# Kernel optimization log

Hardware: AMD Instinct MI355X
Metric: run time of the kernel (lower is better)

## Reference

```python
import jax, jax.numpy as jnp
import numpy as np

N = 50000
E = 800000
D = 256
EPS = 1e-5  # BatchNorm eps


def _gcn_conv(x, W, b, row, col):
    # PyG GCNConv: h = x @ W; add self-loops; sym-normalize; scatter-add; + bias
    h = x @ W  # [N, D]
    deg = jnp.zeros((N,), x.dtype).at[col].add(jnp.ones((row.shape[0],), x.dtype))
    dinv = jax.lax.rsqrt(deg)  # deg >= 1 thanks to self-loops
    norm = dinv[row] * dinv[col]  # [E+N]
    msg = h[row] * norm[:, None]  # gather + scale, [E+N, D]
    out = jnp.zeros_like(h).at[col].add(msg)  # scatter-aggregate
    return out + b


def _bn(x, gamma, beta):
    # BatchNorm1d in training mode: batch statistics over nodes
    m = jnp.mean(x, axis=0)
    v = jnp.var(x, axis=0)
    return (x - m) * jax.lax.rsqrt(v + EPS) * gamma + beta


def setup_inputs() -> dict:
    key = jax.random.key(0)
    ks = jax.random.split(key, 4)
    x = jax.random.normal(ks[0], (N, D), dtype=jnp.float32)
    edge_index = jax.random.randint(ks[1], (2, E), 0, N, dtype=jnp.int64)
    s = 1.0 / np.sqrt(D)
    W1 = jax.random.uniform(ks[2], (D, D), jnp.float32, -s, s)
    W2 = jax.random.uniform(ks[3], (D, D), jnp.float32, -s, s)
    z = jnp.zeros((D,), jnp.float32)
    o = jnp.ones((D,), jnp.float32)
    return {"x": x, "edge_index": edge_index,
            "W1": W1, "b1": z, "g1": o, "be1": z,
            "W2": W2, "b2": z, "g2": o, "be2": z}


def reference(x, edge_index, W1, b1, g1, be1, W2, b2, g2, be2):
    loops = jnp.arange(N, dtype=edge_index.dtype)
    row = jnp.concatenate([edge_index[0], loops])  # sources
    col = jnp.concatenate([edge_index[1], loops])  # targets
    # layer 1: GCNConv -> BN -> ReLU (dropout is identity in eval)
    h = _gcn_conv(x, W1, b1, row, col)
    h = jax.nn.relu(_bn(h, g1, be1))
    # layer 2
    h = _gcn_conv(h, W2, b2, row, col)
    h = jax.nn.relu(_bn(h, g2, be2))
    return h
```

## Files before the change

kernel.cpp:

```cpp
#include <hip/hip_runtime.h>
#include <cstdint>
#include <cstddef>

constexpr int N = 50000;
constexpr int E = 800000;
constexpr int D = 256;
constexpr float EPS = 1e-5f;
constexpr int NB = (N + 255) / 256;
constexpr int GB = (N + 63) / 64;
constexpr int CB = (E + 255) / 256;
constexpr int AGG_BLOCKS = 2048;

constexpr int ZTOT4 = (N * 4 + 4 * D * 4 + 16) / 16;
constexpr int ZBLK = (ZTOT4 + 63) / 64;

typedef __attribute__((ext_vector_type(8))) short short8;
typedef __attribute__((ext_vector_type(4))) float f32x4;

__device__ __forceinline__ unsigned short f2bf(float f) {
  union { float f; unsigned u; } c; c.f = f;
  unsigned u = c.u;
  u += 0x7fff + ((u >> 16) & 1);
  return (unsigned short)(u >> 16);
}
__device__ __forceinline__ float bf2f(unsigned short h) {
  union { unsigned u; float f; } c; c.u = ((unsigned)h) << 16;
  return c.f;
}
__device__ __forceinline__ float bflo(unsigned u) {
  union { unsigned x; float f; } c; c.x = u << 16; return c.f;
}
__device__ __forceinline__ float bfhi(unsigned u) {
  union { unsigned x; float f; } c; c.x = u & 0xffff0000u; return c.f;
}
__device__ __forceinline__ unsigned cvt_pk(float lo, float hi) {
  unsigned r;
  asm("v_cvt_pk_bf16_f32 %0, %1, %2" : "=v"(r) : "v"(lo), "v"(hi));
  return r;
}
__device__ __forceinline__ int2 ldnt_pair(const int2* p) {
  unsigned long long v = __builtin_nontemporal_load((const unsigned long long*)p);
  int2 r;
  r.x = (int)(unsigned)(v & 0xffffffffull);
  r.y = (int)(unsigned)(v >> 32);
  return r;
}

__device__ __forceinline__ int detect64(const void* ei) {
  const int* p = (const int*)ei;
  int l = threadIdx.x & 63;
  int nz = (p[2 * l + 1] != 0) | (p[2 * l + 129] != 0);
  return __ballot(nz) == 0ULL;
}

__device__ __forceinline__ int edge_at(const void* ei, int is64, long long pos) {
  if (is64) return (int)((const long long*)ei)[pos];
  return ((const int*)ei)[pos];
}

template <bool A_BF16, bool FUSE_BN>
__device__ __forceinline__ void gemm_body(const void* __restrict__ Ap,
                                          const unsigned short* __restrict__ Wf,
                                          unsigned short* __restrict__ C,
                                          const float* __restrict__ sc,
                                          const float* __restrict__ sh,
                                          int bid) {
  __shared__ unsigned short As[64][264];
  int t = threadIdx.x;
  int lane = t & 63;
  int w = t >> 6;
  int row0 = bid * 64;
  int l16 = lane & 15, lk = lane >> 4;

  f32x4 acc[4][4];
#pragma unroll
  for (int i = 0; i < 4; ++i)
#pragma unroll
    for (int j = 0; j < 4; ++j) acc[i][j] = (f32x4){0.f, 0.f, 0.f, 0.f};

  int arow = t >> 2;
  int ak0 = (t & 3) * 8;
  int gr = row0 + arow;
  bool inb = (gr < N);

#pragma unroll
  for (int ks = 0; ks < 8; ++ks) {
    int kc = ks * 32 + ak0;
    float f[8] = {0.f, 0.f, 0.f, 0.f, 0.f, 0.f, 0.f, 0.f};
    if (inb) {
      if (A_BF16) {
        const unsigned short* A = (const unsigned short*)Ap;
        short8 v = *(const short8*)&A[(size_t)gr * 256 + kc];
#pragma unroll
        for (int j = 0; j < 8; ++j) f[j] = bf2f((unsigned short)v[j]);
      } else {
        const float* A = (const float*)Ap;
        float4 f0 = *(const float4*)&A[(size_t)gr * 256 + kc];
        float4 f1 = *(const float4*)&A[(size_t)gr * 256 + kc + 4];
        f[0] = f0.x; f[1] = f0.y; f[2] = f0.z; f[3] = f0.w;
        f[4] = f1.x; f[5] = f1.y; f[6] = f1.z; f[7] = f1.w;
      }
    }
    if (FUSE_BN) {
#pragma unroll
      for (int j = 0; j < 8; ++j)
        f[j] = fmaxf(fmaf(f[j], sc[kc + j], sh[kc + j]), 0.f);
    }
    uint4 pk;
    pk.x = cvt_pk(f[0], f[1]);
    pk.y = cvt_pk(f[2], f[3]);
    pk.z = cvt_pk(f[4], f[5]);
    pk.w = cvt_pk(f[6], f[7]);
    *(uint4*)&As[arow][kc] = pk;
  }
  __syncthreads();

#pragma unroll
  for (int ks = 0; ks < 8; ++ks) {
    short8 af[4];
#pragma unroll
    for (int mf = 0; mf < 4; ++mf)
      af[mf] = *(const short8*)&As[mf * 16 + l16][ks * 32 + lk * 8];
#pragma unroll
    for (int nf = 0; nf < 4; ++nf) {
      short8 bf = *(const short8*)&Wf[(((size_t)ks * 16 + w * 4 + nf) * 64 + lane) * 8];
#pragma unroll
      for (int mf = 0; mf < 4; ++mf)
        acc[mf][nf] = __builtin_amdgcn_mfma_f32_16x16x32_bf16(af[mf], bf, acc[mf][nf], 0, 0, 0);
    }
  }
  __syncthreads();

  unsigned short(*Cs)[264] = As;
#pragma unroll
  for (int mf = 0; mf < 4; ++mf)
#pragma unroll
    for (int nf = 0; nf < 4; ++nf)
#pragma unroll
      for (int r = 0; r < 4; ++r)
        Cs[mf * 16 + lk * 4 + r][w * 64 + nf * 16 + l16] = f2bf(acc[mf][nf][r]);
  __syncthreads();
#pragma unroll
  for (int it = 0; it < 8; ++it) {
    int r = it * 8 + (t >> 5);
    int gr2 = row0 + r;
    if (gr2 < N)
      *(short8*)&C[(size_t)gr2 * 256 + (t & 31) * 8] = *(const short8*)&Cs[r][(t & 31) * 8];
  }
}

__global__ __launch_bounds__(256) void k_gemm1_count(const float* __restrict__ x,
                                                     const unsigned short* __restrict__ Wf1,
                                                     unsigned short* __restrict__ hbuf,
                                                     const void* __restrict__ ei,
                                                     int* __restrict__ degc) {
  if (blockIdx.x < GB) {
    gemm_body<false, false>(x, Wf1, hbuf, nullptr, nullptr, blockIdx.x);
  } else {
    int is64 = detect64(ei);
    int e = (blockIdx.x - GB) * 256 + threadIdx.x;
    if (e >= E) return;
    int c = edge_at(ei, is64, (long long)E + e);
    atomicAdd(&degc[c], 1);
  }
}

__global__ __launch_bounds__(256) void k_gemm2(const unsigned short* __restrict__ A,
                                               const unsigned short* __restrict__ Wf,
                                               unsigned short* __restrict__ C,
                                               const float* __restrict__ sc,
                                               const float* __restrict__ sh) {
  gemm_body<true, true>(A, Wf, C, sc, sh, blockIdx.x);
}

__global__ void k_scan_partial(const int* __restrict__ degc, int* __restrict__ bsum,
                               float* __restrict__ dinv) {
  __shared__ int sd[256];
  int t = threadIdx.x;
  int i = blockIdx.x * 256 + t;
  int dv = (i < N) ? degc[i] : 0;
  if (i < N) dinv[i] = rsqrtf((float)(dv + 1));
  int v = (i < N) ? (dv + 1) : 0;
  sd[t] = v;
  __syncthreads();
  for (int s = 128; s > 0; s >>= 1) {
    if (t < s) sd[t] += sd[t + s];
    __syncthreads();
  }
  if (t == 0) bsum[blockIdx.x] = sd[0];
}

__global__ void k_scan_final(const int* __restrict__ degc, const int* __restrict__ bsum,
                             const float* __restrict__ dinv, int* __restrict__ offs,
                             int* __restrict__ curs, int2* __restrict__ epair) {
  __shared__ int sb[256];
  __shared__ int sd[256];
  int t = threadIdx.x;
  int bv = (t < NB) ? bsum[t] : 0;
  sb[t] = bv;
  __syncthreads();
  for (int off = 1; off < 256; off <<= 1) {
    int x = (t >= off) ? sb[t - off] : 0;
    __syncthreads();
    sb[t] += x;
    __syncthreads();
  }
  int base = sb[blockIdx.x] - bsum[blockIdx.x];
  int i = blockIdx.x * 256 + t;
  int v = (i < N) ? (degc[i] + 1) : 0;
  sd[t] = v;
  __syncthreads();
  for (int off = 1; off < 256; off <<= 1) {
    int x = (t >= off) ? sd[t - off] : 0;
    __syncthreads();
    sd[t] += x;
    __syncthreads();
  }
  if (i < N) {
    int o = base + sd[t] - v;
    offs[i] = o;
    curs[i] = o + 1;
    float d = dinv[i];
    epair[o] = make_int2(i, __float_as_int(d * d));
  }
  if (i == N - 1) offs[N] = base + sd[t];
}

__global__ void k_fill_edges(const void* __restrict__ ei,
                             const float* __restrict__ dinv, int* __restrict__ curs,
                             int2* __restrict__ epair) {
  int is64 = detect64(ei);
  int e = blockIdx.x * 256 + threadIdx.x;
  if (e >= E) return;
  int r = edge_at(ei, is64, e);
  int c = edge_at(ei, is64, (long long)E + e);
  int p = atomicAdd(&curs[c], 1);
  epair[p] = make_int2(r, __float_as_int(dinv[r] * dinv[c]));
}

__global__ void k_wfrag(const float* __restrict__ W1, const float* __restrict__ W2,
                        unsigned short* __restrict__ Wf1, unsigned short* __restrict__ Wf2,
                        int4* __restrict__ zbase) {
  int b = blockIdx.x;
  if (b >= 256) {
    int idx4 = (b - 256) * 64 + threadIdx.x;
    if (idx4 < ZTOT4) zbase[idx4] = make_int4(0, 0, 0, 0);
    return;
  }
  const float* W = (b < 128) ? W1 : W2;
  unsigned short* Wf = (b < 128) ? Wf1 : Wf2;
  int tile = b & 127;
  int lane = threadIdx.x;
  int kstep = tile >> 4, wn = tile & 15;
  int kbase = kstep * 32 + (lane >> 4) * 8;
  int col = wn * 16 + (lane & 15);
  float f[8];
#pragma unroll
  for (int j = 0; j < 8; ++j) f[j] = W[(size_t)(kbase + j) * 256 + col];
  uint4 pk;
  pk.x = cvt_pk(f[0], f[1]);
  pk.y = cvt_pk(f[2], f[3]);
  pk.z = cvt_pk(f[4], f[5]);
  pk.w = cvt_pk(f[6], f[7]);
  *(uint4*)&Wf[(((size_t)tile) * 64 + lane) * 8] = pk;
}

__global__ __launch_bounds__(256) void k_agg(const unsigned short* __restrict__ h,
                                             const int* __restrict__ offs,
                                             const int2* __restrict__ epair,
                                             const float* __restrict__ bias,
                                             unsigned short* __restrict__ outp,
                                             float* __restrict__ partial) {
  int t = threadIdx.x;
  int wv = t >> 6;
  int lane = t & 63;
  float4 bb = ((const float4*)bias)[lane];
  float s0 = 0.f, s1 = 0.f, s2 = 0.f, s3 = 0.f;
  float q0 = 0.f, q1 = 0.f, q2 = 0.f, q3 = 0.f;

#define ACC4(v, wgt)                         \
  do {                                       \
    a0 = fmaf(wgt, bflo((v).x), a0);         \
    a1 = fmaf(wgt, bfhi((v).x), a1);         \
    a2 = fmaf(wgt, bflo((v).y), a2);         \
    a3 = fmaf(wgt, bfhi((v).y), a3);         \
  } while (0)

  for (int nd0 = blockIdx.x * 4; nd0 < N; nd0 += AGG_BLOCKS * 4) {
    int nd = nd0 + wv;
    if (nd < N) {
      int node = __builtin_amdgcn_readfirstlane(nd);
      int e = offs[node];
      int end = offs[node + 1];
      float a0 = 0.f, a1 = 0.f, a2 = 0.f, a3 = 0.f;

      for (; e + 8 <= end; e += 8) {
        int2 p0 = ldnt_pair(&epair[e + 0]), p1 = ldnt_pair(&epair[e + 1]);
        int2 p2 = ldnt_pair(&epair[e + 2]), p3 = ldnt_pair(&epair[e + 3]);
        int2 p4 = ldnt_pair(&epair[e + 4]), p5 = ldnt_pair(&epair[e + 5]);
        int2 p6 = ldnt_pair(&epair[e + 6]), p7 = ldnt_pair(&epair[e + 7]);
        uint2 v0 = *(const uint2*)&h[(size_t)p0.x * 256 + lane * 4];
        uint2 v1 = *(const uint2*)&h[(size_t)p1.x * 256 + lane * 4];
        uint2 v2 = *(const uint2*)&h[(size_t)p2.x * 256 + lane * 4];
        uint2 v3 = *(const uint2*)&h[(size_t)p3.x * 256 + lane * 4];
        uint2 v4 = *(const uint2*)&h[(size_t)p4.x * 256 + lane * 4];
        uint2 v5 = *(const uint2*)&h[(size_t)p5.x * 256 + lane * 4];
        uint2 v6 = *(const uint2*)&h[(size_t)p6.x * 256 + lane * 4];
        uint2 v7 = *(const uint2*)&h[(size_t)p7.x * 256 + lane * 4];
        ACC4(v0, __int_as_float(p0.y));
        ACC4(v1, __int_as_float(p1.y));
        ACC4(v2, __int_as_float(p2.y));
        ACC4(v3, __int_as_float(p3.y));
        ACC4(v4, __int_as_float(p4.y));
        ACC4(v5, __int_as_float(p5.y));
        ACC4(v6, __int_as_float(p6.y));
        ACC4(v7, __int_as_float(p7.y));
      }
      if (e < end) {
#pragma unroll
        for (int k = 0; k < 8; ++k) {
          int idx = e + k;
          bool act = (idx < end);
          int2 p = ldnt_pair(&epair[act ? idx : end - 1]);
          float wgt = act ? __int_as_float(p.y) : 0.f;
          uint2 v = *(const uint2*)&h[(size_t)p.x * 256 + lane * 4];
          ACC4(v, wgt);
        }
      }

      uint2 ov;
      ov.x = cvt_pk(a0 + bb.x, a1 + bb.y);
      ov.y = cvt_pk(a2 + bb.z, a3 + bb.w);
      *(uint2*)&outp[(size_t)nd * 256 + lane * 4] = ov;
      float f0 = bflo(ov.x), f1 = bfhi(ov.x), f2v = bflo(ov.y), f3 = bfhi(ov.y);
      s0 += f0; q0 = fmaf(f0, f0, q0);
      s1 += f1; q1 = fmaf(f1, f1, q1);
      s2 += f2v; q2 = fmaf(f2v, f2v, q2);
      s3 += f3; q3 = fmaf(f3, f3, q3);
    }
  }
#undef ACC4

  __shared__ float4 ps[256];
  __shared__ float4 pq[256];
  ps[t] = {s0, s1, s2, s3};
  pq[t] = {q0, q1, q2, q3};
  __syncthreads();
  float* pout = partial + (size_t)blockIdx.x * 512;
  if (t < 64) {
    float4 a = ps[t], b = ps[64 + t], c = ps[128 + t], d = ps[192 + t];
    float4 o = {a.x + b.x + c.x + d.x, a.y + b.y + c.y + d.y,
                a.z + b.z + c.z + d.z, a.w + b.w + c.w + d.w};
    ((float4*)pout)[t] = o;
  } else if (t < 128) {
    int l = t - 64;
    float4 a = pq[l], b = pq[64 + l], c = pq[128 + l], d = pq[192 + l];
    float4 o = {a.x + b.x + c.x + d.x, a.y + b.y + c.y + d.y,
                a.z + b.z + c.z + d.z, a.w + b.w + c.w + d.w};
    ((float4*)(pout + 256))[l] = o;
  }
}

__global__ __launch_bounds__(256) void k_bnred(const float* __restrict__ partial,
                                               float* __restrict__ bnsum,
                                               float* __restrict__ bnsq,
                                               int* __restrict__ cnt,
                                               const float* __restrict__ g,
                                               const float* __restrict__ be,
                                               float* __restrict__ sc,
                                               float* __restrict__ sh) {
  int t = threadIdx.x;
  float s = 0.f, q = 0.f;
  int b0 = blockIdx.x * (AGG_BLOCKS / 16);
  for (int b = b0; b < b0 + AGG_BLOCKS / 16; ++b) {
    s += partial[(size_t)b * 512 + t];
    q += partial[(size_t)b * 512 + 256 + t];
  }
  atomicAdd(&bnsum[t], s);
  atomicAdd(&bnsq[t], q);
  __threadfence();
  __shared__ int last;
  if (t == 0) last = (atomicAdd(cnt, 1) == 15);
  __syncthreads();
  if (last) {
    float S = atomicAdd(&bnsum[t], 0.f);
    float Q = atomicAdd(&bnsq[t], 0.f);
    const float inv = 1.f / (float)N;
    float m = S * inv;
    float v = Q * inv - m * m;
    float sf = rsqrtf(v + EPS) * g[t];
    sc[t] = sf;
    sh[t] = be[t] - m * sf;
  }
}

__global__ __launch_bounds__(256) void k_bnapply(const unsigned short* __restrict__ in,
                                                 float* __restrict__ outp,
                                                 const float* __restrict__ sc,
                                                 const float* __restrict__ sh) {
  int t = threadIdx.x;
  int lane = t & 63;
  int sub = t >> 6;
  float4 s4 = ((const float4*)sc)[lane];
  float4 h4 = ((const float4*)sh)[lane];
  for (int r = blockIdx.x * 4 + sub; r < N; r += gridDim.x * 4) {
    uint2 u = *(const uint2*)&in[(size_t)r * 256 + lane * 4];
    float4 v;
    v.x = fmaxf(fmaf(bflo(u.x), s4.x, h4.x), 0.f);
    v.y = fmaxf(fmaf(bfhi(u.x), s4.y, h4.y), 0.f);
    v.z = fmaxf(fmaf(bflo(u.y), s4.z, h4.z), 0.f);
    v.w = fmaxf(fmaf(bfhi(u.y), s4.w, h4.w), 0.f);
    *(float4*)&outp[(size_t)r * 256 + lane * 4] = v;
  }
}

extern "C" void kernel_launch(void* const* d_in, const int* in_sizes, int n_in,
                              void* d_out, int out_size, void* d_ws, size_t ws_size,
                              hipStream_t stream) {
  const float* x  = (const float*)d_in[0];
  const void*  ei = d_in[1];
  const float* W1 = (const float*)d_in[2];
  const float* b1 = (const float*)d_in[3];
  const float* g1 = (const float*)d_in[4];
  const float* be1 = (const float*)d_in[5];
  const float* W2 = (const float*)d_in[6];
  const float* b2 = (const float*)d_in[7];
  const float* g2 = (const float*)d_in[8];
  const float* be2 = (const float*)d_in[9];
  float* out = (float*)d_out;

  char* base = (char*)d_ws;
  size_t off = 0;
  unsigned short* hbuf = (unsigned short*)(base + off); off += (size_t)N * D * 2;
  unsigned short* abuf = (unsigned short*)(base + off); off += (size_t)N * D * 2;
  unsigned short* Wf1 = (unsigned short*)(base + off);  off += (size_t)D * D * 2;
  unsigned short* Wf2 = (unsigned short*)(base + off);  off += (size_t)D * D * 2;
  int*   degc = (int*)(base + off);    off += (size_t)N * 4;
  float* bnsum1 = (float*)(base + off); off += (size_t)D * 4;
  float* bnsq1  = (float*)(base + off); off += (size_t)D * 4;
  float* bnsum2 = (float*)(base + off); off += (size_t)D * 4;
  float* bnsq2  = (float*)(base + off); off += (size_t)D * 4;
  int*   cnt1 = (int*)(base + off);    off += 8;
  int*   cnt2 = (int*)(base + off);    off += 8;
  float* dinv = (float*)(base + off); off += (size_t)N * 4;
  int*   offs = (int*)(base + off);   off += (size_t)(N + 4) * 4;
  int*   curs = (int*)(base + off);   off += (size_t)N * 4;
  int2*  epair = (int2*)(base + off); off += (size_t)(E + N) * 8;
  float* partial = (float*)(base + off); off += (size_t)AGG_BLOCKS * 512 * 4;
  float* sc1 = (float*)(base + off);  off += (size_t)D * 4;
  float* sh1 = (float*)(base + off);  off += (size_t)D * 4;
  float* sc2 = (float*)(base + off);  off += (size_t)D * 4;
  float* sh2 = (float*)(base + off);  off += (size_t)D * 4;
  int*   bsum = (int*)(base + off);   off += 256 * 4;

  k_wfrag<<<256 + ZBLK, 64, 0, stream>>>(W1, W2, Wf1, Wf2, (int4*)degc);

  k_gemm1_count<<<GB + CB, 256, 0, stream>>>(x, Wf1, hbuf, ei, degc);

  k_scan_partial<<<NB, 256, 0, stream>>>(degc, bsum, dinv);
  k_scan_final<<<NB, 256, 0, stream>>>(degc, bsum, dinv, offs, curs, epair);
  k_fill_edges<<<CB, 256, 0, stream>>>(ei, dinv, curs, epair);

  k_agg<<<AGG_BLOCKS, 256, 0, stream>>>(hbuf, offs, epair, b1, abuf, partial);
  k_bnred<<<16, 256, 0, stream>>>(partial, bnsum1, bnsq1, cnt1, g1, be1, sc1, sh1);

  k_gemm2<<<GB, 256, 0, stream>>>(abuf, Wf2, hbuf, sc1, sh1);
  k_agg<<<AGG_BLOCKS, 256, 0, stream>>>(hbuf, offs, epair, b2, abuf, partial);
  k_bnred<<<16, 256, 0, stream>>>(partial, bnsum2, bnsq2, cnt2, g2, be2, sc2, sh2);
  k_bnapply<<<512, 256, 0, stream>>>(abuf, out, sc2, sh2);
}
```

Baseline: 280.4 us.

## Merge scan kernels with grid barrier and move degree count into wfrag

Replaces the zeroing blocks with hipMemsetAsync and moves the degree-count atomics into the weight-fragment kernel, so GEMM1 runs alone. The two scan kernels are merged into one with a spin-wait grid barrier on a done counter, which removes a launch and reuses the computed dinv. The final BN-apply output uses nontemporal stores. The spin barrier assumes all NB (196) blocks are co-resident, which holds on this GPU but is fragile. The done counter sits inside the memset range so it is reset on every call.

```diff
diff --git a/kernel.cpp b/kernel.cpp
--- a/kernel.cpp
+++ b/kernel.cpp
@@ -9,10 +9,8 @@
 constexpr int NB = (N + 255) / 256;
 constexpr int GB = (N + 63) / 64;
 constexpr int CB = (E + 255) / 256;
+constexpr int CB64 = (E + 63) / 64;
 constexpr int AGG_BLOCKS = 2048;
-
-constexpr int ZTOT4 = (N * 4 + 4 * D * 4 + 16) / 16;
-constexpr int ZBLK = (ZTOT4 + 63) / 64;
 
 typedef __attribute__((ext_vector_type(8))) short short8;
 typedef __attribute__((ext_vector_type(4))) float f32x4;
@@ -149,20 +147,10 @@
   }
 }
 
-__global__ __launch_bounds__(256) void k_gemm1_count(const float* __restrict__ x,
-                                                     const unsigned short* __restrict__ Wf1,
-                                                     unsigned short* __restrict__ hbuf,
-                                                     const void* __restrict__ ei,
-                                                     int* __restrict__ degc) {
-  if (blockIdx.x < GB) {
-    gemm_body<false, false>(x, Wf1, hbuf, nullptr, nullptr, blockIdx.x);
-  } else {
-    int is64 = detect64(ei);
-    int e = (blockIdx.x - GB) * 256 + threadIdx.x;
-    if (e >= E) return;
-    int c = edge_at(ei, is64, (long long)E + e);
-    atomicAdd(&degc[c], 1);
-  }
+__global__ __launch_bounds__(256) void k_gemm1(const float* __restrict__ x,
+                                               const unsigned short* __restrict__ Wf,
+                                               unsigned short* __restrict__ C) {
+  gemm_body<false, false>(x, Wf, C, nullptr, nullptr, blockIdx.x);
 }
 
 __global__ __launch_bounds__(256) void k_gemm2(const unsigned short* __restrict__ A,
@@ -173,29 +161,67 @@
   gemm_body<true, true>(A, Wf, C, sc, sh, blockIdx.x);
 }
 
-__global__ void k_scan_partial(const int* __restrict__ degc, int* __restrict__ bsum,
-                               float* __restrict__ dinv) {
+__global__ __launch_bounds__(64) void k_wfrag_count(
+    const float* __restrict__ W1, const float* __restrict__ W2,
+    unsigned short* __restrict__ Wf1, unsigned short* __restrict__ Wf2,
+    const void* __restrict__ ei, int* __restrict__ degc) {
+  int b = blockIdx.x;
+  if (b >= 256) {
+    int is64 = detect64(ei);
+    int e = (b - 256) * 64 + threadIdx.x;
+    if (e >= E) return;
+    int c = edge_at(ei, is64, (long long)E + e);
+    atomicAdd(&degc[c], 1);
+    return;
+  }
+  const float* W = (b < 128) ? W1 : W2;
+  unsigned short* Wf = (b < 128) ? Wf1 : Wf2;
+  int tile = b & 127;
+  int lane = threadIdx.x;
+  int kstep = tile >> 4, wn = tile & 15;
+  int kbase = kstep * 32 + (lane >> 4) * 8;
+  int col = wn * 16 + (lane & 15);
+  float f[8];
+#pragma unroll
+  for (int j = 0; j < 8; ++j) f[j] = W[(size_t)(kbase + j) * 256 + col];
+  uint4 pk;
+  pk.x = cvt_pk(f[0], f[1]);
+  pk.y = cvt_pk(f[2], f[3]);
+  pk.z = cvt_pk(f[4], f[5]);
+  pk.w = cvt_pk(f[6], f[7]);
+  *(uint4*)&Wf[(((size_t)tile) * 64 + lane) * 8] = pk;
+}
+
+__global__ __launch_bounds__(256) void k_scan(const int* __restrict__ degc,
+                                              float* __restrict__ dinv,
+                                              int* __restrict__ offs,
+                                              int* __restrict__ curs,
+                                              int2* __restrict__ epair,
+                                              int* __restrict__ bsum,
+                                              int* __restrict__ done) {
   __shared__ int sd[256];
+  __shared__ int sb[256];
   int t = threadIdx.x;
   int i = blockIdx.x * 256 + t;
   int dv = (i < N) ? degc[i] : 0;
-  if (i < N) dinv[i] = rsqrtf((float)(dv + 1));
+  float di = rsqrtf((float)(dv + 1));
+  if (i < N) dinv[i] = di;
   int v = (i < N) ? (dv + 1) : 0;
+
   sd[t] = v;
   __syncthreads();
   for (int s = 128; s > 0; s >>= 1) {
     if (t < s) sd[t] += sd[t + s];
     __syncthreads();
   }
-  if (t == 0) bsum[blockIdx.x] = sd[0];
-}
-
-__global__ void k_scan_final(const int* __restrict__ degc, const int* __restrict__ bsum,
-                             const float* __restrict__ dinv, int* __restrict__ offs,
-                             int* __restrict__ curs, int2* __restrict__ epair) {
-  __shared__ int sb[256];
-  __shared__ int sd[256];
-  int t = threadIdx.x;
+  if (t == 0) {
+    bsum[blockIdx.x] = sd[0];
+    __threadfence();
+    atomicAdd(done, 1);
+    while (atomicAdd(done, 0) < NB) { __builtin_amdgcn_s_sleep(1); }
+  }
+  __syncthreads();
+
   int bv = (t < NB) ? bsum[t] : 0;
   sb[t] = bv;
   __syncthreads();
@@ -206,8 +232,7 @@
     __syncthreads();
   }
   int base = sb[blockIdx.x] - bsum[blockIdx.x];
-  int i = blockIdx.x * 256 + t;
-  int v = (i < N) ? (degc[i] + 1) : 0;
+
   sd[t] = v;
   __syncthreads();
   for (int off = 1; off < 256; off <<= 1) {
@@ -220,8 +245,7 @@
     int o = base + sd[t] - v;
     offs[i] = o;
     curs[i] = o + 1;
-    float d = dinv[i];
-    epair[o] = make_int2(i, __float_as_int(d * d));
+    epair[o] = make_int2(i, __float_as_int(di * di));
   }
   if (i == N - 1) offs[N] = base + sd[t];
 }
@@ -236,33 +260,6 @@
   int c = edge_at(ei, is64, (long long)E + e);
   int p = atomicAdd(&curs[c], 1);
   epair[p] = make_int2(r, __float_as_int(dinv[r] * dinv[c]));
-}
-
-__global__ void k_wfrag(const float* __restrict__ W1, const float* __restrict__ W2,
-                        unsigned short* __restrict__ Wf1, unsigned short* __restrict__ Wf2,
-                        int4* __restrict__ zbase) {
-  int b = blockIdx.x;
-  if (b >= 256) {
-    int idx4 = (b - 256) * 64 + threadIdx.x;
-    if (idx4 < ZTOT4) zbase[idx4] = make_int4(0, 0, 0, 0);
-    return;
-  }
-  const float* W = (b < 128) ? W1 : W2;
-  unsigned short* Wf = (b < 128) ? Wf1 : Wf2;
-  int tile = b & 127;
-  int lane = threadIdx.x;
-  int kstep = tile >> 4, wn = tile & 15;
-  int kbase = kstep * 32 + (lane >> 4) * 8;
-  int col = wn * 16 + (lane & 15);
-  float f[8];
-#pragma unroll
-  for (int j = 0; j < 8; ++j) f[j] = W[(size_t)(kbase + j) * 256 + col];
-  uint4 pk;
-  pk.x = cvt_pk(f[0], f[1]);
-  pk.y = cvt_pk(f[2], f[3]);
-  pk.z = cvt_pk(f[4], f[5]);
-  pk.w = cvt_pk(f[6], f[7]);
-  *(uint4*)&Wf[(((size_t)tile) * 64 + lane) * 8] = pk;
 }
 
 __global__ __launch_bounds__(256) void k_agg(const unsigned short* __restrict__ h,
@@ -405,12 +402,12 @@
   float4 h4 = ((const float4*)sh)[lane];
   for (int r = blockIdx.x * 4 + sub; r < N; r += gridDim.x * 4) {
     uint2 u = *(const uint2*)&in[(size_t)r * 256 + lane * 4];
-    float4 v;
-    v.x = fmaxf(fmaf(bflo(u.x), s4.x, h4.x), 0.f);
-    v.y = fmaxf(fmaf(bfhi(u.x), s4.y, h4.y), 0.f);
-    v.z = fmaxf(fmaf(bflo(u.y), s4.z, h4.z), 0.f);
-    v.w = fmaxf(fmaf(bfhi(u.y), s4.w, h4.w), 0.f);
-    *(float4*)&outp[(size_t)r * 256 + lane * 4] = v;
+    f32x4 v;
+    v[0] = fmaxf(fmaf(bflo(u.x), s4.x, h4.x), 0.f);
+    v[1] = fmaxf(fmaf(bfhi(u.x), s4.y, h4.y), 0.f);
+    v[2] = fmaxf(fmaf(bflo(u.y), s4.z, h4.z), 0.f);
+    v[3] = fmaxf(fmaf(bfhi(u.y), s4.w, h4.w), 0.f);
+    __builtin_nontemporal_store(v, (f32x4*)&outp[(size_t)r * 256 + lane * 4]);
   }
 }
 
@@ -440,8 +437,10 @@
   float* bnsq1  = (float*)(base + off); off += (size_t)D * 4;
   float* bnsum2 = (float*)(base + off); off += (size_t)D * 4;
   float* bnsq2  = (float*)(base + off); off += (size_t)D * 4;
-  int*   cnt1 = (int*)(base + off);    off += 8;
-  int*   cnt2 = (int*)(base + off);    off += 8;
+  int*   cnt1 = (int*)(base + off);    off += 4;
+  int*   cnt2 = (int*)(base + off);    off += 4;
+  int*   sdone = (int*)(base + off);   off += 8;
+  size_t zero_bytes = (size_t)N * 4 + 4 * (size_t)D * 4 + 16;
   float* dinv = (float*)(base + off); off += (size_t)N * 4;
   int*   offs = (int*)(base + off);   off += (size_t)(N + 4) * 4;
   int*   curs = (int*)(base + off);   off += (size_t)N * 4;
@@ -453,12 +452,13 @@
   float* sh2 = (float*)(base + off);  off += (size_t)D * 4;
   int*   bsum = (int*)(base + off);   off += 256 * 4;
 
-  k_wfrag<<<256 + ZBLK, 64, 0, stream>>>(W1, W2, Wf1, Wf2, (int4*)degc);
-
-  k_gemm1_count<<<GB + CB, 256, 0, stream>>>(x, Wf1, hbuf, ei, degc);
-
-  k_scan_partial<<<NB, 256, 0, stream>>>(degc, bsum, dinv);
-  k_scan_final<<<NB, 256, 0, stream>>>(degc, bsum, dinv, offs, curs, epair);
+  (void)hipMemsetAsync(degc, 0, zero_bytes, stream);
+
+  k_wfrag_count<<<256 + CB64, 64, 0, stream>>>(W1, W2, Wf1, Wf2, ei, degc);
+
+  k_gemm1<<<GB, 256, 0, stream>>>(x, Wf1, hbuf);
+
+  k_scan<<<NB, 256, 0, stream>>>(degc, dinv, offs, curs, epair, bsum, sdone);
   k_fill_edges<<<CB, 256, 0, stream>>>(ei, dinv, curs, epair);
 
   k_agg<<<AGG_BLOCKS, 256, 0, stream>>>(hbuf, offs, epair, b1, abuf, partial);
```

New measurement: 306.9 us. 1.09x slower.
